# Performance work log

Hardware: AMD Instinct MI355X
Metric: run time of the kernel (lower is better)

Reference implementation:

```python
import jax, jax.numpy as jnp
import numpy as np

HEAD_DIM = 64
NUM_Q_HEADS = 16
NUM_KV_HEADS = 4
MIN_TS = 1.0
MAX_TS = 10000.0


def _timescale(d):
    frac = 2.0 * jnp.arange(d // 2, dtype=jnp.float32) / d
    return MIN_TS * (MAX_TS / MIN_TS) ** frac  # [d/2]


def _rope(v, pos):
    # v: [B,S,H,D] float, pos: [B,S] int
    ts = _timescale(v.shape[-1])
    sinu = pos[:, :, None, None].astype(jnp.float32) / ts  # [B,S,1,D/2]
    sin, cos = jnp.sin(sinu), jnp.cos(sinu)
    x1, x2 = jnp.split(v.astype(jnp.float32), 2, axis=-1)
    return jnp.concatenate([x1 * cos - x2 * sin, x2 * cos + x1 * sin], axis=-1)


def setup_inputs() -> dict:
    key = jax.random.key(0)
    ks = jax.random.split(key, 5)
    B, S, E = 2, 2048, 1024
    Hq, Hk, D = NUM_Q_HEADS, NUM_KV_HEADS, HEAD_DIM
    sc = 0.02
    x = jax.random.normal(ks[0], (B, S, E), dtype=jnp.float32)
    q_pos = jnp.broadcast_to(jnp.arange(S, dtype=jnp.int32), (B, S))
    Wq = jax.random.normal(ks[1], (E, Hq * D), dtype=jnp.float32) * sc
    Wk = jax.random.normal(ks[2], (E, Hk * D), dtype=jnp.float32) * sc
    Wv = jax.random.normal(ks[3], (E, Hk * D), dtype=jnp.float32) * sc
    Wo = jax.random.normal(ks[4], (Hq * D, E), dtype=jnp.float32) * sc
    return {"x": x, "q_pos": q_pos, "Wq": Wq, "Wk": Wk, "Wv": Wv, "Wo": Wo}


def reference(x, q_pos, Wq, Wk, Wv, Wo):
    B, S, E = x.shape
    Hq, Hk, D = NUM_Q_HEADS, NUM_KV_HEADS, HEAD_DIM
    G = Hq // Hk  # gqa groups

    q = (x @ Wq).reshape(B, S, Hq, D)
    k = (x @ Wk).reshape(B, S, Hk, D)
    v = (x @ Wv).reshape(B, S, Hk, D)

    q = _rope(q, q_pos)  # kv_pos defaults to q_pos
    k = _rope(k, q_pos)

    # [B,Hk,G,S,D] grouped query heads vs shared kv heads
    qg = q.transpose(0, 2, 1, 3).reshape(B, Hk, G, S, D)
    kt = k.transpose(0, 2, 1, 3)  # [B,Hk,S,D]
    vt = v.transpose(0, 2, 1, 3)

    # NOTE: original uses scale=1.0 (no 1/sqrt(D))
    scores = jnp.einsum('bhgqd,bhkd->bhgqk', qg, kt)
    probs = jax.nn.softmax(scores, axis=-1)
    out = jnp.einsum('bhgqk,bhkd->bhgqd', probs, vt)  # [B,Hk,G,S,D]
    out = out.reshape(B, Hq, S, D).transpose(0, 2, 1, 3).reshape(B, S, Hq * D)
    return out @ Wo
```

## Files before the change

### kernel.cpp

```cpp
#include <hip/hip_runtime.h>
#include <hip/hip_fp16.h>
#include <math.h>

typedef __attribute__((ext_vector_type(8))) _Float16 half8;
typedef __attribute__((ext_vector_type(4))) _Float16 half4;
typedef __attribute__((ext_vector_type(4))) float f32x4;
typedef __attribute__((ext_vector_type(16))) float f32x16;
typedef __attribute__((ext_vector_type(4))) unsigned uint4v;

#define HQ 16
#define HK 4
#define DH 64
#define NB 2
#define SEQ 2048
#define EDIM 1024
#define KD 1024

__device__ __forceinline__ void gload16(const void* g, void* l) {
  __builtin_amdgcn_global_load_lds(
      (const __attribute__((address_space(1))) void*)g,
      (__attribute__((address_space(3))) void*)l, 16, 0, 0);
}

__global__ __launch_bounds__(256) void prep_cvt_rope(
    const float* __restrict__ x, _Float16* __restrict__ xh,
    const int* __restrict__ qpos, float2* __restrict__ tab) {
  int bx = blockIdx.x;
  int tid = threadIdx.x;
  if (bx < 4096) {
    int i = bx * 256 + tid;
    float4 v = ((const float4*)x)[i];
    half4 h;
    h[0] = (_Float16)v.x; h[1] = (_Float16)v.y; h[2] = (_Float16)v.z; h[3] = (_Float16)v.w;
    *(half4*)(xh + (size_t)i * 4) = h;
  } else {
    int i = (bx - 4096) * 256 + tid;
    int row = i >> 5, d = i & 31;
    float ang = (float)qpos[row] * expf((float)d * -0.2878231366242558f);
    float sn, cs;
    sincosf(ang, &sn, &cs);
    tab[i] = make_float2(sn, cs);
  }
}

__global__ __launch_bounds__(256) void transpose_w4(
    const float* __restrict__ Wq, const float* __restrict__ Wk,
    const float* __restrict__ Wv, const float* __restrict__ Wo,
    _Float16* __restrict__ WT, _Float16* __restrict__ WoT) {
  int z = blockIdx.z;
  const float* W;
  _Float16* dst;
  int N, roff;
  if (z == 0)      { W = Wq; N = 1024; roff = 0;    dst = WT; }
  else if (z == 1) { W = Wk; N = 256;  roff = 1024; dst = WT;  if (blockIdx.x >= 4) return; }
  else if (z == 2) { W = Wv; N = 256;  roff = 1280; dst = WT;  if (blockIdx.x >= 4) return; }
  else             { W = Wo; N = 1024; roff = 0;    dst = WoT; }

  __shared__ float t[64][65];
  int n0 = blockIdx.x * 64, k0 = blockIdx.y * 64;
  int tid = threadIdx.x;
#pragma unroll
  for (int p = 0; p < 4; ++p) {
    int idx = tid + p * 256;
    int r = idx >> 4;
    int c4 = idx & 15;
    float4 v = *(const float4*)(W + (size_t)(k0 + r) * N + n0 + c4 * 4);
    t[r][c4 * 4 + 0] = v.x; t[r][c4 * 4 + 1] = v.y;
    t[r][c4 * 4 + 2] = v.z; t[r][c4 * 4 + 3] = v.w;
  }
  __syncthreads();
#pragma unroll
  for (int p = 0; p < 4; ++p) {
    int idx = tid + p * 256;
    int n = idx >> 4;
    int k4 = idx & 15;
    half4 h;
    h[0] = (_Float16)t[k4 * 4 + 0][n]; h[1] = (_Float16)t[k4 * 4 + 1][n];
    h[2] = (_Float16)t[k4 * 4 + 2][n]; h[3] = (_Float16)t[k4 * 4 + 3][n];
    *(half4*)(dst + (size_t)(roff + n0 + n) * KD + k0 + k4 * 4) = h;
  }
}

__global__ __launch_bounds__(256) void transpose_v_kernel(const _Float16* __restrict__ vhp,
                                                          _Float16* __restrict__ vtp) {
  __shared__ _Float16 t[64][72];
  int bh = blockIdx.y;
  int s0 = blockIdx.x * 64;
  const _Float16* src = vhp + ((size_t)bh * SEQ + s0) * DH;
  _Float16* dst = vtp + (size_t)bh * DH * SEQ + s0;
  int tid = threadIdx.x;
#pragma unroll
  for (int p = 0; p < 2; ++p) {
    int idx = tid + p * 256;
    int r = idx >> 3, c8 = idx & 7;
    half8 v = *(const half8*)(src + (size_t)r * DH + c8 * 8);
#pragma unroll
    for (int i = 0; i < 8; ++i) t[r][c8 * 8 + i] = v[i];
  }
  __syncthreads();
#pragma unroll
  for (int p = 0; p < 2; ++p) {
    int idx = tid + p * 256;
    int d = idx >> 3, c8 = idx & 7;
    half8 v;
#pragma unroll
    for (int i = 0; i < 8; ++i) v[i] = t[c8 * 8 + i][d];
    *(half8*)(dst + (size_t)d * SEQ + c8 * 8) = v;
  }
}

#define SWZ(r, kb) ((kb) ^ (((r) & 7) << 4))

__global__ __launch_bounds__(256) void gemm_qkv_rope(
    const _Float16* __restrict__ xh, const _Float16* __restrict__ WT,
    const float2* __restrict__ rtab,
    _Float16* __restrict__ qh, _Float16* __restrict__ kh, _Float16* __restrict__ vh) {
  __shared__ char As[64 * 64 * 2];
  __shared__ char Bs[128 * 64 * 2];
  int tid = threadIdx.x, lane = tid & 63, wid = tid >> 6;
  int wr = wid >> 1, wc = wid & 1;
  int bm = blockIdx.x, bn = blockIdx.y;

  const char* Ag = (const char*)(xh + (size_t)bm * 64 * KD);
  const char* Bg = (const char*)(WT + (size_t)bn * 128 * KD);

  int colS = 16 * ((lane & 7) ^ (lane >> 3));
  int rS = (lane >> 3);

  f32x4 acc[2][4] = {};

  for (int kt = 0; kt < KD / 64; ++kt) {
#pragma unroll
    for (int p = 0; p < 2; ++p) {
      int sb = wid * 2 + p;
      int r = sb * 8 + rS;
      gload16(Ag + (size_t)r * (KD * 2) + kt * 128 + colS, As + sb * 1024);
    }
#pragma unroll
    for (int p = 0; p < 4; ++p) {
      int sb = wid * 4 + p;
      int r = sb * 8 + rS;
      gload16(Bg + (size_t)r * (KD * 2) + kt * 128 + colS, Bs + sb * 1024);
    }
    __syncthreads();
#pragma unroll
    for (int kk = 0; kk < 2; ++kk) {
      int kb = kk * 64 + (lane >> 4) * 16;
      half8 af[2], bf[4];
#pragma unroll
      for (int mf = 0; mf < 2; ++mf) {
        int r = wr * 32 + mf * 16 + (lane & 15);
        af[mf] = *(const half8*)(As + r * 128 + SWZ(r, kb));
      }
#pragma unroll
      for (int nf = 0; nf < 4; ++nf) {
        int r = wc * 64 + nf * 16 + (lane & 15);
        bf[nf] = *(const half8*)(Bs + r * 128 + SWZ(r, kb));
      }
#pragma unroll
      for (int mf = 0; mf < 2; ++mf)
#pragma unroll
        for (int nf = 0; nf < 4; ++nf)
          acc[mf][nf] = __builtin_amdgcn_mfma_f32_16x16x32_f16(af[mf], bf[nf], acc[mf][nf], 0, 0, 0);
    }
    __syncthreads();
  }

  int col0 = bn * 128 + wc * 64;
  int row_base = bm * 64 + wr * 32;
#pragma unroll
  for (int mf = 0; mf < 2; ++mf) {
#pragma unroll
    for (int j = 0; j < 4; ++j) {
      int row = row_base + mf * 16 + (lane >> 4) * 4 + j;
      int b = row >> 11, s = row & (SEQ - 1);
      if (col0 < 1024) {
        int hq = col0 >> 6;
        size_t base = (((size_t)b * HQ + hq) * SEQ + s) * DH;
#pragma unroll
        for (int nf = 0; nf < 2; ++nf) {
          int d = nf * 16 + (lane & 15);
          float2 scv = rtab[row * 32 + d];
          float x1 = acc[mf][nf][j], x2 = acc[mf][nf + 2][j];
          qh[base + d]      = (_Float16)(x1 * scv.y - x2 * scv.x);
          qh[base + d + 32] = (_Float16)(x2 * scv.y + x1 * scv.x);
        }
      } else if (col0 < 1280) {
        int hk = (col0 - 1024) >> 6;
        size_t base = (((size_t)b * HK + hk) * SEQ + s) * DH;
#pragma unroll
        for (int nf = 0; nf < 2; ++nf) {
          int d = nf * 16 + (lane & 15);
          float2 scv = rtab[row * 32 + d];
          float x1 = acc[mf][nf][j], x2 = acc[mf][nf + 2][j];
          kh[base + d]      = (_Float16)(x1 * scv.y - x2 * scv.x);
          kh[base + d + 32] = (_Float16)(x2 * scv.y + x1 * scv.x);
        }
      } else {
        int hk = (col0 - 1280) >> 6;
        size_t base = (((size_t)b * HK + hk) * SEQ + s) * DH;
#pragma unroll
        for (int nf = 0; nf < 4; ++nf) {
          int d = nf * 16 + (lane & 15);
          vh[base + d] = (_Float16)acc[mf][nf][j];
        }
      }
    }
  }
}

__global__ __launch_bounds__(256) void attn_kernel(
    const _Float16* __restrict__ qh, const _Float16* __restrict__ kh,
    const _Float16* __restrict__ vt, _Float16* __restrict__ oh) {
  __shared__ char Ks[2][128 * 64 * 2];
  __shared__ char Vs[2][64 * 128 * 2];

  int tid = threadIdx.x, lane = tid & 63, wid = tid >> 6;
  int half = lane >> 5, l31 = lane & 31;
  bool lopart = (half == 0);
  int qt = blockIdx.x, bh = blockIdx.y;
  int b = bh >> 4, hq = bh & 15, hk = hq >> 2;

  const _Float16* Qg = qh + (((size_t)b * HQ + hq) * SEQ + qt * 128 + wid * 32 + l31) * DH;
  const char* Kg = (const char*)(kh + (((size_t)b * HK + hk) * SEQ) * DH);
  const char* Vtg = (const char*)(vt + (size_t)(b * HK + hk) * DH * SEQ);

  const _Float16 l2e = (_Float16)1.44269504f;
  half8 qf[4];
#pragma unroll
  for (int ks = 0; ks < 4; ++ks) {
    half8 q0 = *(const half8*)(Qg + ks * 16 + half * 8);
#pragma unroll
    for (int i = 0; i < 8; ++i) q0[i] = q0[i] * l2e;
    qf[ks] = q0;
  }

  int colK = 16 * ((lane & 7) ^ (lane >> 3));
  int rK = lane >> 3;

  f32x16 oacc[2] = {};
  float m = -3e38f, l = 0.f;

#pragma unroll
  for (int p = 0; p < 4; ++p) {
    int r = (wid * 4 + p) * 8 + rK;
    gload16(Kg + (size_t)r * 128 + colK, Ks[0] + (wid * 4 + p) * 1024);
    int d = (wid * 4 + p) * 4 + (lane >> 4);
    int colV = ((lane & 15) * 16) ^ ((d & 7) << 4);
    gload16(Vtg + (size_t)d * (SEQ * 2) + colV, Vs[0] + (wid * 4 + p) * 1024);
  }

  int cur = 0;
  for (int kt = 0; kt < SEQ / 128; ++kt) {
    if (kt + 1 < SEQ / 128) {
#pragma unroll
      for (int p = 0; p < 4; ++p) {
        int r = (wid * 4 + p) * 8 + rK;
        gload16(Kg + (size_t)((kt + 1) * 128 + r) * 128 + colK,
                Ks[cur ^ 1] + (wid * 4 + p) * 1024);
        int d = (wid * 4 + p) * 4 + (lane >> 4);
        int colV = ((lane & 15) * 16) ^ ((d & 7) << 4);
        gload16(Vtg + (size_t)d * (SEQ * 2) + (kt + 1) * 256 + colV,
                Vs[cur ^ 1] + (wid * 4 + p) * 1024);
      }
      asm volatile("s_waitcnt vmcnt(8)" ::: "memory");
    } else {
      asm volatile("s_waitcnt vmcnt(0)" ::: "memory");
    }
    __builtin_amdgcn_s_barrier();
    const char* KsB = Ks[cur];
    const char* VsB = Vs[cur];

    f32x16 sacc[4] = {};
    __builtin_amdgcn_s_setprio(1);
#pragma unroll
    for (int b4 = 0; b4 < 4; ++b4) {
      int r = b4 * 32 + l31;
#pragma unroll
      for (int ks = 0; ks < 4; ++ks) {
        half8 kf = *(const half8*)(KsB + r * 128 + SWZ(r, ks * 32 + half * 16));
        sacc[b4] = __builtin_amdgcn_mfma_f32_32x32x16_f16(kf, qf[ks], sacc[b4], 0, 0, 0);
      }
    }
    __builtin_amdgcn_s_setprio(0);

    float pm = sacc[0][0];
#pragma unroll
    for (int b4 = 0; b4 < 4; ++b4)
#pragma unroll
      for (int r = 0; r < 16; ++r)
        if (b4 || r) pm = fmaxf(pm, sacc[b4][r]);
    pm = fmaxf(pm, __shfl_xor(pm, 32, 64));
    float mnew = fmaxf(m, pm);
    float alpha = __builtin_amdgcn_exp2f(m - mnew);
    m = mnew;
    oacc[0] *= alpha;
    oacc[1] *= alpha;
    l *= alpha;
    float ps = 0.f;

#pragma unroll
    for (int b4 = 0; b4 < 4; ++b4) {
      float e[16];
#pragma unroll
      for (int r = 0; r < 16; ++r) {
        e[r] = __builtin_amdgcn_exp2f(sacc[b4][r] - m);
        ps += e[r];
      }
      unsigned W0[4], W1[4];
#pragma unroll
      for (int qd = 0; qd < 4; ++qd) {
        W0[qd] = __builtin_bit_cast(unsigned, __builtin_amdgcn_cvt_pkrtz(e[4 * qd + 0], e[4 * qd + 1]));
        W1[qd] = __builtin_bit_cast(unsigned, __builtin_amdgcn_cvt_pkrtz(e[4 * qd + 2], e[4 * qd + 3]));
      }
      half8 pf[2];
#pragma unroll
      for (int s = 0; s < 2; ++s) {
        unsigned selA = lopart ? W0[2 * s + 1] : W0[2 * s];
        unsigned crA = (unsigned)__shfl_xor((int)selA, 32, 64);
        unsigned selB = lopart ? W1[2 * s + 1] : W1[2 * s];
        unsigned crB = (unsigned)__shfl_xor((int)selB, 32, 64);
        uint4v u;
        u[0] = lopart ? W0[2 * s] : crA;
        u[1] = lopart ? W1[2 * s] : crB;
        u[2] = lopart ? crA : W0[2 * s + 1];
        u[3] = lopart ? crB : W1[2 * s + 1];
        pf[s] = __builtin_bit_cast(half8, u);
      }
      __builtin_amdgcn_s_setprio(1);
#pragma unroll
      for (int s = 0; s < 2; ++s) {
        int kvb = b4 * 64 + s * 32 + half * 16;
#pragma unroll
        for (int dblk = 0; dblk < 2; ++dblk) {
          int d = dblk * 32 + l31;
          half8 vf = *(const half8*)(VsB + d * 256 + SWZ(d, kvb));
          oacc[dblk] = __builtin_amdgcn_mfma_f32_32x32x16_f16(vf, pf[s], oacc[dblk], 0, 0, 0);
        }
      }
      __builtin_amdgcn_s_setprio(0);
    }
    ps += __shfl_xor(ps, 32, 64);
    l += ps;
    __builtin_amdgcn_s_barrier();
    cur ^= 1;
  }

  int s = qt * 128 + wid * 32 + l31;
  float invl = 1.f / l;
  size_t base = ((size_t)b * SEQ + s) * 1024 + hq * 64;
#pragma unroll
  for (int dblk = 0; dblk < 2; ++dblk) {
#pragma unroll
    for (int qd = 0; qd < 4; ++qd) {
      half4 o;
#pragma unroll
      for (int j = 0; j < 4; ++j) o[j] = (_Float16)(oacc[dblk][qd * 4 + j] * invl);
      *(half4*)(oh + base + dblk * 32 + qd * 8 + half * 4) = o;
    }
  }
}

__global__ __launch_bounds__(256) void gemm_out(
    const _Float16* __restrict__ ah, const _Float16* __restrict__ WoT,
    float* __restrict__ out) {
  __shared__ char As[64 * 64 * 2];
  __shared__ char Bs[128 * 64 * 2];
  int tid = threadIdx.x, lane = tid & 63, wid = tid >> 6;
  int wr = wid >> 1, wc = wid & 1;
  int bm = blockIdx.x, bn = blockIdx.y;
  const char* Ag = (const char*)(ah + (size_t)bm * 64 * KD);
  const char* Bg = (const char*)(WoT + (size_t)bn * 128 * KD);
  int colS = 16 * ((lane & 7) ^ (lane >> 3));
  int rS = (lane >> 3);
  f32x4 acc[2][4] = {};

  for (int kt = 0; kt < KD / 64; ++kt) {
#pragma unroll
    for (int p = 0; p < 2; ++p) {
      int sb = wid * 2 + p;
      int r = sb * 8 + rS;
      gload16(Ag + (size_t)r * (KD * 2) + kt * 128 + colS, As + sb * 1024);
    }
#pragma unroll
    for (int p = 0; p < 4; ++p) {
      int sb = wid * 4 + p;
      int r = sb * 8 + rS;
      gload16(Bg + (size_t)r * (KD * 2) + kt * 128 + colS, Bs + sb * 1024);
    }
    __syncthreads();
#pragma unroll
    for (int kk = 0; kk < 2; ++kk) {
      int kb = kk * 64 + (lane >> 4) * 16;
      half8 af[2], bf[4];
#pragma unroll
      for (int mf = 0; mf < 2; ++mf) {
        int r = wr * 32 + mf * 16 + (lane & 15);
        af[mf] = *(const half8*)(As + r * 128 + SWZ(r, kb));
      }
#pragma unroll
      for (int nf = 0; nf < 4; ++nf) {
        int r = wc * 64 + nf * 16 + (lane & 15);
        bf[nf] = *(const half8*)(Bs + r * 128 + SWZ(r, kb));
      }
#pragma unroll
      for (int mf = 0; mf < 2; ++mf)
#pragma unroll
        for (int nf = 0; nf < 4; ++nf)
          acc[mf][nf] = __builtin_amdgcn_mfma_f32_16x16x32_f16(af[mf], bf[nf], acc[mf][nf], 0, 0, 0);
    }
    __syncthreads();
  }

  int row0 = bm * 64 + wr * 32, col0 = bn * 128 + wc * 64;
#pragma unroll
  for (int mf = 0; mf < 2; ++mf)
#pragma unroll
    for (int j = 0; j < 4; ++j) {
      int row = row0 + mf * 16 + (lane >> 4) * 4 + j;
#pragma unroll
      for (int nf = 0; nf < 4; ++nf)
        out[(size_t)row * 1024 + col0 + nf * 16 + (lane & 15)] = acc[mf][nf][j];
    }
}

extern "C" void kernel_launch(void* const* d_in, const int* in_sizes, int n_in,
                              void* d_out, int out_size, void* d_ws, size_t ws_size,
                              hipStream_t stream) {
  const float* x  = (const float*)d_in[0];
  const int* qpos = (const int*)d_in[1];
  const float* Wq = (const float*)d_in[2];
  const float* Wk = (const float*)d_in[3];
  const float* Wv = (const float*)d_in[4];
  const float* Wo = (const float*)d_in[5];
  float* out = (float*)d_out;

  char* ws = (char*)d_ws;
  _Float16* xh  = (_Float16*)(ws);
  _Float16* WT  = (_Float16*)(ws + 8388608);
  _Float16* WoT = (_Float16*)(ws + 11534336);
  _Float16* qhp = (_Float16*)(ws + 13631488);
  _Float16* khp = (_Float16*)(ws + 22020096);
  _Float16* vhp = (_Float16*)(ws + 24117248);
  _Float16* ohp = (_Float16*)(ws + 26214400);
  float2*   rtab = (float2*)(ws + 34603008);
  _Float16* vtp = (_Float16*)(ws + 35651584);

  prep_cvt_rope<<<4608, 256, 0, stream>>>(x, xh, qpos, rtab);
  transpose_w4<<<dim3(16, 16, 4), 256, 0, stream>>>(Wq, Wk, Wv, Wo, WT, WoT);
  gemm_qkv_rope<<<dim3(64, 12), 256, 0, stream>>>(xh, WT, rtab, qhp, khp, vhp);
  transpose_v_kernel<<<dim3(32, 8), 256, 0, stream>>>(vhp, vtp);
  attn_kernel<<<dim3(16, 32), 256, 0, stream>>>(qhp, khp, vtp, ohp);
  gemm_out<<<dim3(64, 8), 256, 0, stream>>>(ohp, WoT, out);
}
```

Before: 109.2 us.

## Single-buffer K/V tiles in attention and shorten max/sum reduction chains

Replaces the double-buffered K/V LDS staging and its explicit prefetch with a single buffer that is loaded at the start of each iteration and guarded by __syncthreads. This halves the kernel's LDS footprint, likely so more blocks fit per CU and the added waves hide load latency. The row-max and exp-sum reductions are also restructured into trees and four partial accumulators to shorten dependency chains. In exchange, global-to-LDS loads no longer overlap with compute inside a block, which exposes load latency unless occupancy makes up for it.

```diff
diff --git a/kernel.cpp b/kernel.cpp
--- a/kernel.cpp
+++ b/kernel.cpp
@@ -212,8 +212,8 @@
 __global__ __launch_bounds__(256) void attn_kernel(
     const _Float16* __restrict__ qh, const _Float16* __restrict__ kh,
     const _Float16* __restrict__ vt, _Float16* __restrict__ oh) {
-  __shared__ char Ks[2][128 * 64 * 2];
-  __shared__ char Vs[2][64 * 128 * 2];
+  __shared__ char Ks[128 * 64 * 2];
+  __shared__ char Vs[64 * 128 * 2];
 
   int tid = threadIdx.x, lane = tid & 63, wid = tid >> 6;
   int half = lane >> 5, l31 = lane & 31;
@@ -241,35 +241,16 @@
   f32x16 oacc[2] = {};
   float m = -3e38f, l = 0.f;
 
-#pragma unroll
-  for (int p = 0; p < 4; ++p) {
-    int r = (wid * 4 + p) * 8 + rK;
-    gload16(Kg + (size_t)r * 128 + colK, Ks[0] + (wid * 4 + p) * 1024);
-    int d = (wid * 4 + p) * 4 + (lane >> 4);
-    int colV = ((lane & 15) * 16) ^ ((d & 7) << 4);
-    gload16(Vtg + (size_t)d * (SEQ * 2) + colV, Vs[0] + (wid * 4 + p) * 1024);
-  }
-
-  int cur = 0;
   for (int kt = 0; kt < SEQ / 128; ++kt) {
-    if (kt + 1 < SEQ / 128) {
-#pragma unroll
-      for (int p = 0; p < 4; ++p) {
-        int r = (wid * 4 + p) * 8 + rK;
-        gload16(Kg + (size_t)((kt + 1) * 128 + r) * 128 + colK,
-                Ks[cur ^ 1] + (wid * 4 + p) * 1024);
-        int d = (wid * 4 + p) * 4 + (lane >> 4);
-        int colV = ((lane & 15) * 16) ^ ((d & 7) << 4);
-        gload16(Vtg + (size_t)d * (SEQ * 2) + (kt + 1) * 256 + colV,
-                Vs[cur ^ 1] + (wid * 4 + p) * 1024);
-      }
-      asm volatile("s_waitcnt vmcnt(8)" ::: "memory");
-    } else {
-      asm volatile("s_waitcnt vmcnt(0)" ::: "memory");
-    }
-    __builtin_amdgcn_s_barrier();
-    const char* KsB = Ks[cur];
-    const char* VsB = Vs[cur];
+#pragma unroll
+    for (int p = 0; p < 4; ++p) {
+      int r = (wid * 4 + p) * 8 + rK;
+      gload16(Kg + (size_t)(kt * 128 + r) * 128 + colK, Ks + (wid * 4 + p) * 1024);
+      int d = (wid * 4 + p) * 4 + (lane >> 4);
+      int colV = ((lane & 15) * 16) ^ ((d & 7) << 4);
+      gload16(Vtg + (size_t)d * (SEQ * 2) + kt * 256 + colV, Vs + (wid * 4 + p) * 1024);
+    }
+    __syncthreads();
 
     f32x16 sacc[4] = {};
     __builtin_amdgcn_s_setprio(1);
@@ -278,18 +259,25 @@
       int r = b4 * 32 + l31;
 #pragma unroll
       for (int ks = 0; ks < 4; ++ks) {
-        half8 kf = *(const half8*)(KsB + r * 128 + SWZ(r, ks * 32 + half * 16));
+        half8 kf = *(const half8*)(Ks + r * 128 + SWZ(r, ks * 32 + half * 16));
         sacc[b4] = __builtin_amdgcn_mfma_f32_32x32x16_f16(kf, qf[ks], sacc[b4], 0, 0, 0);
       }
     }
     __builtin_amdgcn_s_setprio(0);
 
-    float pm = sacc[0][0];
-#pragma unroll
-    for (int b4 = 0; b4 < 4; ++b4)
-#pragma unroll
-      for (int r = 0; r < 16; ++r)
-        if (b4 || r) pm = fmaxf(pm, sacc[b4][r]);
+    float pmb[4];
+#pragma unroll
+    for (int b4 = 0; b4 < 4; ++b4) {
+      f32x16 v = sacc[b4];
+      float a0 = fmaxf(v[0], v[1]),   a1 = fmaxf(v[2], v[3]);
+      float a2 = fmaxf(v[4], v[5]),   a3 = fmaxf(v[6], v[7]);
+      float a4 = fmaxf(v[8], v[9]),   a5 = fmaxf(v[10], v[11]);
+      float a6 = fmaxf(v[12], v[13]), a7 = fmaxf(v[14], v[15]);
+      float b0 = fmaxf(a0, a1), b1 = fmaxf(a2, a3);
+      float b2 = fmaxf(a4, a5), b3 = fmaxf(a6, a7);
+      pmb[b4] = fmaxf(fmaxf(b0, b1), fmaxf(b2, b3));
+    }
+    float pm = fmaxf(fmaxf(pmb[0], pmb[1]), fmaxf(pmb[2], pmb[3]));
     pm = fmaxf(pm, __shfl_xor(pm, 32, 64));
     float mnew = fmaxf(m, pm);
     float alpha = __builtin_amdgcn_exp2f(m - mnew);
@@ -297,16 +285,19 @@
     oacc[0] *= alpha;
     oacc[1] *= alpha;
     l *= alpha;
-    float ps = 0.f;
+    float ps0 = 0.f, ps1 = 0.f, ps2 = 0.f, ps3 = 0.f;
 
 #pragma unroll
     for (int b4 = 0; b4 < 4; ++b4) {
       float e[16];
 #pragma unroll
-      for (int r = 0; r < 16; ++r) {
-        e[r] = __builtin_amdgcn_exp2f(sacc[b4][r] - m);
-        ps += e[r];
-      }
+      for (int r = 0; r < 4; ++r)  { e[r] = __builtin_amdgcn_exp2f(sacc[b4][r] - m);  ps0 += e[r]; }
+#pragma unroll
+      for (int r = 4; r < 8; ++r)  { e[r] = __builtin_amdgcn_exp2f(sacc[b4][r] - m);  ps1 += e[r]; }
+#pragma unroll
+      for (int r = 8; r < 12; ++r) { e[r] = __builtin_amdgcn_exp2f(sacc[b4][r] - m);  ps2 += e[r]; }
+#pragma unroll
+      for (int r = 12; r < 16; ++r){ e[r] = __builtin_amdgcn_exp2f(sacc[b4][r] - m);  ps3 += e[r]; }
       unsigned W0[4], W1[4];
 #pragma unroll
       for (int qd = 0; qd < 4; ++qd) {
@@ -334,16 +325,16 @@
 #pragma unroll
         for (int dblk = 0; dblk < 2; ++dblk) {
           int d = dblk * 32 + l31;
-          half8 vf = *(const half8*)(VsB + d * 256 + SWZ(d, kvb));
+          half8 vf = *(const half8*)(Vs + d * 256 + SWZ(d, kvb));
           oacc[dblk] = __builtin_amdgcn_mfma_f32_32x32x16_f16(vf, pf[s], oacc[dblk], 0, 0, 0);
         }
       }
       __builtin_amdgcn_s_setprio(0);
     }
+    float ps = (ps0 + ps1) + (ps2 + ps3);
     ps += __shfl_xor(ps, 32, 64);
     l += ps;
-    __builtin_amdgcn_s_barrier();
-    cur ^= 1;
+    __syncthreads();
   }
 
   int s = qt * 128 + wid * 32 + l31;
```

Result: no change. 110.0 us (+0.7%).
